# Performance work log

Hardware: AMD Instinct MI355X
Metric: run time of the kernel (lower is better)

## Reference

```python
import jax, jax.numpy as jnp
import numpy as np

DIM = 1024
HEADS = 16
DIM_HEAD = 64
SEQ = 2048
BATCH = 4
BASE = 10000.0
SCALING = 1.0


def rope_cos_sin(seq_len, dim_head, base=BASE, scaling=SCALING):
    inv_freq = scaling / (base ** (jnp.arange(0, dim_head, 2, dtype=jnp.float32) / dim_head))
    t = jnp.arange(seq_len, dtype=jnp.float32)
    freqs = t[:, None] * inv_freq[None, :]            # [S, d/2]
    emb = jnp.concatenate([freqs, freqs], axis=-1)    # [S, d]
    return jnp.cos(emb), jnp.sin(emb)


def apply_rotary(x, cos, sin):
    # x: [B, H, S, d]; cos/sin: [S, d]
    d2 = x.shape[-1] // 2
    c = cos[None, None, :, :d2]
    s = sin[None, None, :, :d2]
    x1, x2 = x[..., :d2], x[..., d2:]
    return jnp.concatenate([x1 * c - x2 * s, x1 * s + x2 * c], axis=-1)


def setup_inputs() -> dict:
    key = jax.random.key(0)
    ks = jax.random.split(key, 5)
    x = jax.random.normal(ks[0], (BATCH, SEQ, DIM), dtype=jnp.float32)
    inner = HEADS * DIM_HEAD
    w_qkv = jax.random.normal(ks[1], (DIM, inner * 3), dtype=jnp.float32) * (DIM ** -0.5)
    w_out = jax.random.normal(ks[2], (inner, DIM), dtype=jnp.float32) * (inner ** -0.5)
    b_out = jnp.zeros((DIM,), dtype=jnp.float32)
    ln_gamma = jnp.ones((DIM,), dtype=jnp.float32)
    ln_beta = jnp.zeros((DIM,), dtype=jnp.float32)
    return {"x": x, "w_qkv": w_qkv, "w_out": w_out, "b_out": b_out,
            "ln_gamma": ln_gamma, "ln_beta": ln_beta}


def reference(x, w_qkv, w_out, b_out, ln_gamma, ln_beta):
    # LayerNorm
    mu = jnp.mean(x, axis=-1, keepdims=True)
    var = jnp.var(x, axis=-1, keepdims=True)
    xn = (x - mu) * jax.lax.rsqrt(var + 1e-5) * ln_gamma + ln_beta
    # QKV projection (no bias)
    qkv = xn @ w_qkv                                  # [B, S, 3*inner]
    q, k, v = jnp.split(qkv, 3, axis=-1)
    def split_heads(t):
        B, S, _ = t.shape
        return t.reshape(B, S, HEADS, DIM_HEAD).transpose(0, 2, 1, 3)
    q, k, v = split_heads(q), split_heads(k), split_heads(v)  # [B, H, S, d]
    cos, sin = rope_cos_sin(SEQ, DIM_HEAD)
    q = apply_rotary(q, cos, sin)
    k = apply_rotary(k, cos, sin)
    scale = DIM_HEAD ** -0.5
    dots = jnp.einsum('bhid,bhjd->bhij', q, k) * scale  # [B, H, S, S]
    attn = jax.nn.softmax(dots, axis=-1)
    out = jnp.einsum('bhij,bhjd->bhid', attn, v)       # [B, H, S, d]
    B, H, S, d = out.shape
    out = out.transpose(0, 2, 1, 3).reshape(B, S, H * d)
    return out @ w_out + b_out
```

## Files before the change

### kernel.cpp

```cpp
#include <hip/hip_runtime.h>
#include <hip/hip_bf16.h>
#include <math.h>

#define B_ 4
#define S_ 2048
#define D_ 1024
#define H_ 16
#define DH_ 64
#define INNER_ 1024
#define N3_ 3072
#define ROWS_ 8192

typedef __attribute__((ext_vector_type(8))) short short8;
typedef __attribute__((ext_vector_type(8))) _Float16 half8;
typedef __attribute__((ext_vector_type(4))) float f32x4;

#define QSCALE_ (0.125f * 1.44269504088896f)

#if __has_builtin(__builtin_amdgcn_exp2f)
#define EXP2N(x) __builtin_amdgcn_exp2f(x)
#else
#define EXP2N(x) exp2f(x)
#endif

__device__ __forceinline__ ushort f16rne(float x) {
    _Float16 h = (_Float16)x;
    return *reinterpret_cast<ushort*>(&h);
}

__device__ __forceinline__ int swz(int row, int colByte) {
    return row * 128 + (colByte ^ ((row & 7) << 4));
}

__device__ __forceinline__ void xcd_remap(int& bx, int& by) {
    const int gx  = gridDim.x;
    const int nwg = gx * gridDim.y;
    const int bid = blockIdx.y * gx + blockIdx.x;
    const int swzid = (bid & 7) * (nwg >> 3) + (bid >> 3);
    bx = swzid % gx;
    by = swzid / gx;
}

__global__ __launch_bounds__(256) void ln_kernel(const float* __restrict__ x,
                                                 const float* __restrict__ gamma,
                                                 const float* __restrict__ beta,
                                                 ushort* __restrict__ xn_f) {
    const int row = blockIdx.x;
    const int tid = threadIdx.x;
    const float4 v = ((const float4*)(x + (size_t)row * D_))[tid];
    float s  = v.x + v.y + v.z + v.w;
    float ss = v.x * v.x + v.y * v.y + v.z * v.z + v.w * v.w;
    #pragma unroll
    for (int off = 32; off > 0; off >>= 1) {
        s  += __shfl_down(s, off);
        ss += __shfl_down(ss, off);
    }
    __shared__ float red[8];
    const int wave = tid >> 6, lane = tid & 63;
    if (lane == 0) { red[wave] = s; red[4 + wave] = ss; }
    __syncthreads();
    const float S  = red[0] + red[1] + red[2] + red[3];
    const float SS = red[4] + red[5] + red[6] + red[7];
    const float mu  = S * (1.0f / D_);
    const float var = SS * (1.0f / D_) - mu * mu;
    const float rs  = rsqrtf(var + 1e-5f);
    const float4 g  = ((const float4*)gamma)[tid];
    const float4 bb = ((const float4*)beta)[tid];
    const float o0 = (v.x - mu) * rs * g.x + bb.x;
    const float o1 = (v.y - mu) * rs * g.y + bb.y;
    const float o2 = (v.z - mu) * rs * g.z + bb.z;
    const float o3 = (v.w - mu) * rs * g.w + bb.w;
    *(ushort4*)(xn_f + (size_t)row * D_ + tid * 4) =
        make_ushort4(f16rne(o0), f16rne(o1), f16rne(o2), f16rne(o3));
}

__global__ __launch_bounds__(256) void wtrans_kernel(const float* __restrict__ W,
                                                     ushort* __restrict__ Tf,
                                                     int K, int N) {
    __shared__ float tile[64][68];
    const int tid = threadIdx.x;
    const int n0 = blockIdx.x * 64, k0 = blockIdx.y * 64;
    const int kr = tid >> 4, nc = (tid & 15) * 4;
    #pragma unroll
    for (int li = 0; li < 4; ++li) {
        const int k = kr + li * 16;
        *(float4*)&tile[k][nc] = *(const float4*)(W + (size_t)(k0 + k) * N + n0 + nc);
    }
    __syncthreads();
    const int nl = tid >> 2;
    const int ks = (tid & 3) * 16;
    ushort hbuf[16];
    #pragma unroll
    for (int i = 0; i < 16; ++i) hbuf[i] = f16rne(tile[ks + i][nl]);
    ushort* th = Tf + (size_t)(n0 + nl) * K + k0 + ks;
    #pragma unroll
    for (int i = 0; i < 4; ++i)
        *(ushort4*)(th + i * 4) = make_ushort4(hbuf[i*4], hbuf[i*4+1], hbuf[i*4+2], hbuf[i*4+3]);
}

__global__ __launch_bounds__(256) void gemm_f16_kernel(
        const ushort* __restrict__ Af, const ushort* __restrict__ Bf,
        float* __restrict__ C, int M, int N, int K,
        const float* __restrict__ bias) {
    __shared__ __align__(16) ushort As[128 * 64];
    __shared__ __align__(16) ushort Bs[128 * 64];
    const int tid  = threadIdx.x;
    const int lane = tid & 63;
    const int wv   = tid >> 6;
    const int lr = lane & 15, lg = lane >> 4;
    const int wr = wv >> 1, wc = wv & 1;
    int bx, by;
    xcd_remap(bx, by);
    const int m0 = by * 128, n0 = bx * 128;

    f32x4 acc[4][4];
    #pragma unroll
    for (int i = 0; i < 4; ++i)
        #pragma unroll
        for (int j = 0; j < 4; ++j) acc[i][j] = (f32x4){0.f, 0.f, 0.f, 0.f};

    const int sr = tid >> 3;
    const int ss = (tid & 7) * 16;

    for (int k0 = 0; k0 < K; k0 += 64) {
        __syncthreads();
        #pragma unroll
        for (int li = 0; li < 4; ++li) {
            const int r = sr + li * 32;
            const int off = swz(r, ss);
            *(uint4*)((char*)As + off) = *(const uint4*)(Af + (size_t)(m0 + r) * K + k0 + (ss >> 1));
            *(uint4*)((char*)Bs + off) = *(const uint4*)(Bf + (size_t)(n0 + r) * K + k0 + (ss >> 1));
        }
        __syncthreads();
        #pragma unroll
        for (int kc = 0; kc < 2; ++kc) {
            const int cb = kc * 64 + lg * 16;
            half8 a[4], b[4];
            #pragma unroll
            for (int i = 0; i < 4; ++i) {
                a[i] = *(half8*)((char*)As + swz(wr * 64 + i * 16 + lr, cb));
                b[i] = *(half8*)((char*)Bs + swz(wc * 64 + i * 16 + lr, cb));
            }
            __builtin_amdgcn_s_setprio(1);
            #pragma unroll
            for (int mi = 0; mi < 4; ++mi)
                #pragma unroll
                for (int ni = 0; ni < 4; ++ni)
                    acc[mi][ni] = __builtin_amdgcn_mfma_f32_16x16x32_f16(a[mi], b[ni], acc[mi][ni], 0, 0, 0);
            __builtin_amdgcn_s_setprio(0);
        }
    }

    #pragma unroll
    for (int mi = 0; mi < 4; ++mi) {
        #pragma unroll
        for (int rr = 0; rr < 4; ++rr) {
            const int row = m0 + wr * 64 + mi * 16 + lg * 4 + rr;
            float* crow = C + (size_t)row * N + n0 + wc * 64;
            #pragma unroll
            for (int ni = 0; ni < 4; ++ni) {
                const int col = ni * 16 + lr;
                float v = acc[mi][ni][rr];
                if (bias) v += bias[n0 + wc * 64 + col];
                crow[col] = v;
            }
        }
    }
}

__global__ __launch_bounds__(256) void gemm_qkv_rope_kernel(
        const ushort* __restrict__ Af, const ushort* __restrict__ Bf,
        ushort* __restrict__ qkv16, int M, int N, int K,
        const float* __restrict__ cost, const float* __restrict__ sint) {
    __shared__ __align__(16) ushort As[128 * 64];
    __shared__ __align__(16) ushort Bs[128 * 64];
    const int tid  = threadIdx.x;
    const int lane = tid & 63;
    const int wv   = tid >> 6;
    const int lr = lane & 15, lg = lane >> 4;
    const int wr = wv >> 1, wc = wv & 1;
    int bx, by;
    xcd_remap(bx, by);
    const int m0 = by * 128, n0 = bx * 128;

    f32x4 acc[4][4];
    #pragma unroll
    for (int i = 0; i < 4; ++i)
        #pragma unroll
        for (int j = 0; j < 4; ++j) acc[i][j] = (f32x4){0.f, 0.f, 0.f, 0.f};

    const int sr = tid >> 3;
    const int ss = (tid & 7) * 16;

    for (int k0 = 0; k0 < K; k0 += 64) {
        __syncthreads();
        #pragma unroll
        for (int li = 0; li < 4; ++li) {
            const int r = sr + li * 32;
            const int off = swz(r, ss);
            *(uint4*)((char*)As + off) = *(const uint4*)(Af + (size_t)(m0 + r) * K + k0 + (ss >> 1));
            *(uint4*)((char*)Bs + off) = *(const uint4*)(Bf + (size_t)(n0 + r) * K + k0 + (ss >> 1));
        }
        __syncthreads();
        #pragma unroll
        for (int kc = 0; kc < 2; ++kc) {
            const int cb = kc * 64 + lg * 16;
            half8 a[4], b[4];
            #pragma unroll
            for (int i = 0; i < 4; ++i) {
                a[i] = *(half8*)((char*)As + swz(wr * 64 + i * 16 + lr, cb));
                b[i] = *(half8*)((char*)Bs + swz(wc * 64 + i * 16 + lr, cb));
            }
            __builtin_amdgcn_s_setprio(1);
            #pragma unroll
            for (int mi = 0; mi < 4; ++mi)
                #pragma unroll
                for (int ni = 0; ni < 4; ++ni)
                    acc[mi][ni] = __builtin_amdgcn_mfma_f32_16x16x32_f16(a[mi], b[ni], acc[mi][ni], 0, 0, 0);
            __builtin_amdgcn_s_setprio(0);
        }
    }

    const int seg = n0 >> 10;
    const int colbase = (n0 & 1023) + wc * 64;
    #pragma unroll
    for (int mi = 0; mi < 4; ++mi) {
        #pragma unroll
        for (int rr = 0; rr < 4; ++rr) {
            const int row = m0 + wr * 64 + mi * 16 + lg * 4 + rr;
            const int spos = row & (S_ - 1);
            ushort* wrow = qkv16 + (size_t)row * 3072 + seg * 1024 + colbase;
            if (seg < 2) {
                #pragma unroll
                for (int p = 0; p < 2; ++p) {
                    const int d2 = p * 16 + lr;
                    const float c = cost[spos * 32 + d2];
                    const float s = sint[spos * 32 + d2];
                    const float v1 = acc[mi][p][rr];
                    const float v2 = acc[mi][p + 2][rr];
                    float r1 = v1 * c - v2 * s;
                    float r2 = v1 * s + v2 * c;
                    if (seg == 0) { r1 *= QSCALE_; r2 *= QSCALE_; }
                    wrow[p * 16 + lr]      = f16rne(r1);
                    wrow[p * 16 + lr + 32] = f16rne(r2);
                }
            } else {
                #pragma unroll
                for (int ni = 0; ni < 4; ++ni)
                    wrow[ni * 16 + lr] = f16rne(acc[mi][ni][rr]);
            }
        }
    }
}

__global__ __launch_bounds__(256) void rope_table_kernel(float* __restrict__ cost,
                                                         float* __restrict__ sint) {
    const int idx = blockIdx.x * 256 + threadIdx.x;
    const int s = idx >> 5;
    const int i = idx & 31;
    const float inv = powf(10000.0f, -(2.0f * (float)i) / 64.0f);
    const float f = (float)s * inv;
    float sv, cv;
    sincosf(f, &sv, &cv);
    cost[idx] = cv;
    sint[idx] = sv;
}

__global__ __launch_bounds__(256) void attn_mfma_kernel(const ushort* __restrict__ Q16,
                                                        ushort* __restrict__ att_f) {
    __shared__ __align__(16) ushort sK[64 * 64];
    __shared__ __align__(16) ushort sV[64 * 64];
    __shared__ __align__(16) ushort Pb[4][2][16 * 64];

    const int tid  = threadIdx.x;
    const int lane = tid & 63;
    const int wv   = tid >> 6;
    const int lr   = lane & 15;
    const int lg   = lane >> 4;

    const int bh = blockIdx.x;
    const int b  = bh >> 4;
    const int h  = bh & 15;
    const int q0 = blockIdx.y * 128;

    half8 q[2][2];
    #pragma unroll
    for (int qt = 0; qt < 2; ++qt) {
        const int qrow = q0 + wv * 32 + qt * 16 + lr;
        const ushort* qp = Q16 + (size_t)(b * S_ + qrow) * 3072 + h * 64;
        #pragma unroll
        for (int kc = 0; kc < 2; ++kc)
            q[qt][kc] = *(const half8*)(qp + kc * 32 + lg * 8);
    }

    half8 onesf;
    #pragma unroll
    for (int i = 0; i < 8; ++i) onesf[i] = (lr == 0) ? (_Float16)1.0f : (_Float16)0.0f;

    f32x4 accO[2][4];
    #pragma unroll
    for (int qt = 0; qt < 2; ++qt)
        #pragma unroll
        for (int t = 0; t < 4; ++t) accO[qt][t] = (f32x4){0.f, 0.f, 0.f, 0.f};
    f32x4 accL[2];
    accL[0] = (f32x4){0.f, 0.f, 0.f, 0.f};
    accL[1] = (f32x4){0.f, 0.f, 0.f, 0.f};

    const int kr0 = tid >> 3, ksl = tid & 7;
    const int vjp = tid & 31;
    const int vd  = (tid >> 5) * 8;

    const ushort* kvbase = Q16 + (size_t)(b * S_) * 3072 + h * 64;

    short8 rk0, rk1, rv0, rv1;

#define LOADT(J0)                                                              \
    {                                                                          \
        const ushort* ktb = kvbase + (size_t)(J0) * 3072 + 1024;               \
        rk0 = *(const short8*)(ktb + (size_t)kr0 * 3072 + ksl * 8);            \
        rk1 = *(const short8*)(ktb + (size_t)(kr0 + 32) * 3072 + ksl * 8);     \
        const ushort* vtb = kvbase + (size_t)(J0) * 3072 + 2048;               \
        rv0 = *(const short8*)(vtb + (size_t)(2 * vjp) * 3072 + vd);           \
        rv1 = *(const short8*)(vtb + (size_t)(2 * vjp + 1) * 3072 + vd);       \
    }

#define WRITET()                                                               \
    {                                                                          \
        *(short8*)((char*)sK + swz(kr0, ksl * 16)) = rk0;                      \
        *(short8*)((char*)sK + swz(kr0 + 32, ksl * 16)) = rk1;                 \
        _Pragma("unroll")                                                      \
        for (int i = 0; i < 8; ++i) {                                          \
            const int off = swz(vd + i, vjp * 4);                              \
            *(uint*)((char*)sV + off) = (uint)(ushort)rv0[i] | ((uint)(ushort)rv1[i] << 16); \
        }                                                                      \
    }

    LOADT(0)
    WRITET()

    const int NT = S_ / 64;
    for (int t = 0; t < NT; ++t) {
        __syncthreads();
        if (t + 1 < NT) LOADT((t + 1) * 64)

        f32x4 accS[2][4];
        #pragma unroll
        for (int qt = 0; qt < 2; ++qt)
            #pragma unroll
            for (int tt = 0; tt < 4; ++tt) accS[qt][tt] = (f32x4){0.f, 0.f, 0.f, 0.f};
        #pragma unroll
        for (int kc = 0; kc < 2; ++kc) {
            #pragma unroll
            for (int tt = 0; tt < 4; ++tt) {
                const int off = swz(tt * 16 + lr, (kc * 32 + lg * 8) * 2);
                half8 kv = *(half8*)((char*)sK + off);
                #pragma unroll
                for (int qt = 0; qt < 2; ++qt)
                    accS[qt][tt] = __builtin_amdgcn_mfma_f32_16x16x32_f16(q[qt][kc], kv, accS[qt][tt], 0, 0, 0);
            }
        }

        #pragma unroll
        for (int qt = 0; qt < 2; ++qt) {
            #pragma unroll
            for (int tt = 0; tt < 4; ++tt)
                #pragma unroll
                for (int r = 0; r < 4; ++r) {
                    const float pv = EXP2N(accS[qt][tt][r]);
                    const int off = swz(lg * 4 + r, (tt * 16 + lr) * 2);
                    *(ushort*)((char*)Pb[wv][qt] + off) = f16rne(pv);
                }
        }

        #pragma unroll
        for (int jc = 0; jc < 2; ++jc) {
            const int aoff = swz(lr, (jc * 32 + lg * 8) * 2);
            half8 pa0 = *(half8*)((char*)Pb[wv][0] + aoff);
            half8 pa1 = *(half8*)((char*)Pb[wv][1] + aoff);
            accL[0] = __builtin_amdgcn_mfma_f32_16x16x32_f16(pa0, onesf, accL[0], 0, 0, 0);
            accL[1] = __builtin_amdgcn_mfma_f32_16x16x32_f16(pa1, onesf, accL[1], 0, 0, 0);
            #pragma unroll
            for (int dt = 0; dt < 4; ++dt) {
                const int boff = swz(dt * 16 + lr, (jc * 32 + lg * 8) * 2);
                half8 vvf = *(half8*)((char*)sV + boff);
                accO[0][dt] = __builtin_amdgcn_mfma_f32_16x16x32_f16(pa0, vvf, accO[0][dt], 0, 0, 0);
                accO[1][dt] = __builtin_amdgcn_mfma_f32_16x16x32_f16(pa1, vvf, accO[1][dt], 0, 0, 0);
            }
        }

        __syncthreads();
        if (t + 1 < NT) WRITET()
    }

    #pragma unroll
    for (int qt = 0; qt < 2; ++qt) {
        #pragma unroll
        for (int r = 0; r < 4; ++r) {
            const float L = __shfl(accL[qt][r], lane & 48);
            const float inv_l = 1.0f / L;
            const int q_ = q0 + wv * 32 + qt * 16 + lg * 4 + r;
            const size_t ob = ((size_t)(b * S_ + q_)) * INNER_ + h * 64;
            #pragma unroll
            for (int dt = 0; dt < 4; ++dt)
                att_f[ob + dt * 16 + lr] = f16rne(accO[qt][dt][r] * inv_l);
        }
    }
#undef LOADT
#undef WRITET
}

extern "C" void kernel_launch(void* const* d_in, const int* in_sizes, int n_in,
                              void* d_out, int out_size, void* d_ws, size_t ws_size,
                              hipStream_t stream) {
    const float* x        = (const float*)d_in[0];
    const float* w_qkv    = (const float*)d_in[1];
    const float* w_out    = (const float*)d_in[2];
    const float* b_out    = (const float*)d_in[3];
    const float* ln_gamma = (const float*)d_in[4];
    const float* ln_beta  = (const float*)d_in[5];
    float* out = (float*)d_out;

    char* wsb = (char*)d_ws;
    ushort* qkv16 = (ushort*)wsb;
    ushort* xn_f  = (ushort*)(wsb + 100663296);
    ushort* att_f = xn_f;
    ushort* wqT_f = (ushort*)(wsb + 134217728);
    ushort* woT_f = (ushort*)(wsb + 134217728 + 8388608);
    float*  cost  = (float*)(wsb + 146800640);
    float*  sint  = cost + S_ * 32;

    ln_kernel<<<ROWS_, 256, 0, stream>>>(x, ln_gamma, ln_beta, xn_f);

    wtrans_kernel<<<dim3(N3_ / 64, D_ / 64), 256, 0, stream>>>(w_qkv, wqT_f, D_, N3_);
    rope_table_kernel<<<(S_ * 32) / 256, 256, 0, stream>>>(cost, sint);

    gemm_qkv_rope_kernel<<<dim3(N3_ / 128, ROWS_ / 128), 256, 0, stream>>>(
        xn_f, wqT_f, qkv16, ROWS_, N3_, D_, cost, sint);

    attn_mfma_kernel<<<dim3(B_ * H_, S_ / 128), 256, 0, stream>>>(qkv16, att_f);

    wtrans_kernel<<<dim3(D_ / 64, D_ / 64), 256, 0, stream>>>(w_out, woT_f, D_, D_);

    gemm_f16_kernel<<<dim3(D_ / 128, ROWS_ / 128), 256, 0, stream>>>(
        att_f, woT_f, out, ROWS_, D_, INNER_, b_out);
}
```

Baseline: 254.5 us.

## Keep attention probabilities in registers by computing transposed S via swapped MFMA operands

After: 235.8 us. 7.3% less time.

```diff
diff --git a/kernel.cpp b/kernel.cpp
--- a/kernel.cpp
+++ b/kernel.cpp
@@ -13,6 +13,7 @@
 
 typedef __attribute__((ext_vector_type(8))) short short8;
 typedef __attribute__((ext_vector_type(8))) _Float16 half8;
+typedef __attribute__((ext_vector_type(4))) _Float16 half4;
 typedef __attribute__((ext_vector_type(4))) float f32x4;
 
 #define QSCALE_ (0.125f * 1.44269504088896f)
@@ -270,7 +271,6 @@
                                                         ushort* __restrict__ att_f) {
     __shared__ __align__(16) ushort sK[64 * 64];
     __shared__ __align__(16) ushort sV[64 * 64];
-    __shared__ __align__(16) ushort Pb[4][2][16 * 64];
 
     const int tid  = threadIdx.x;
     const int lane = tid & 63;
@@ -293,18 +293,12 @@
             q[qt][kc] = *(const half8*)(qp + kc * 32 + lg * 8);
     }
 
-    half8 onesf;
-    #pragma unroll
-    for (int i = 0; i < 8; ++i) onesf[i] = (lr == 0) ? (_Float16)1.0f : (_Float16)0.0f;
-
     f32x4 accO[2][4];
     #pragma unroll
     for (int qt = 0; qt < 2; ++qt)
         #pragma unroll
         for (int t = 0; t < 4; ++t) accO[qt][t] = (f32x4){0.f, 0.f, 0.f, 0.f};
-    f32x4 accL[2];
-    accL[0] = (f32x4){0.f, 0.f, 0.f, 0.f};
-    accL[1] = (f32x4){0.f, 0.f, 0.f, 0.f};
+    float lrun[2] = {0.f, 0.f};
 
     const int kr0 = tid >> 3, ksl = tid & 7;
     const int vjp = tid & 31;
@@ -356,35 +350,37 @@
                 half8 kv = *(half8*)((char*)sK + off);
                 #pragma unroll
                 for (int qt = 0; qt < 2; ++qt)
-                    accS[qt][tt] = __builtin_amdgcn_mfma_f32_16x16x32_f16(q[qt][kc], kv, accS[qt][tt], 0, 0, 0);
-            }
-        }
-
+                    accS[qt][tt] = __builtin_amdgcn_mfma_f32_16x16x32_f16(kv, q[qt][kc], accS[qt][tt], 0, 0, 0);
+            }
+        }
+
+        half4 pf[2][4];
         #pragma unroll
         for (int qt = 0; qt < 2; ++qt) {
-            #pragma unroll
-            for (int tt = 0; tt < 4; ++tt)
-                #pragma unroll
-                for (int r = 0; r < 4; ++r) {
-                    const float pv = EXP2N(accS[qt][tt][r]);
-                    const int off = swz(lg * 4 + r, (tt * 16 + lr) * 2);
-                    *(ushort*)((char*)Pb[wv][qt] + off) = f16rne(pv);
-                }
-        }
-
-        #pragma unroll
-        for (int jc = 0; jc < 2; ++jc) {
-            const int aoff = swz(lr, (jc * 32 + lg * 8) * 2);
-            half8 pa0 = *(half8*)((char*)Pb[wv][0] + aoff);
-            half8 pa1 = *(half8*)((char*)Pb[wv][1] + aoff);
-            accL[0] = __builtin_amdgcn_mfma_f32_16x16x32_f16(pa0, onesf, accL[0], 0, 0, 0);
-            accL[1] = __builtin_amdgcn_mfma_f32_16x16x32_f16(pa1, onesf, accL[1], 0, 0, 0);
+            float ls = 0.f;
+            #pragma unroll
+            for (int tt = 0; tt < 4; ++tt) {
+                const float p0 = EXP2N(accS[qt][tt][0]);
+                const float p1 = EXP2N(accS[qt][tt][1]);
+                const float p2 = EXP2N(accS[qt][tt][2]);
+                const float p3 = EXP2N(accS[qt][tt][3]);
+                ls += (p0 + p1) + (p2 + p3);
+                half4 pk;
+                pk[0] = (_Float16)p0; pk[1] = (_Float16)p1;
+                pk[2] = (_Float16)p2; pk[3] = (_Float16)p3;
+                pf[qt][tt] = pk;
+            }
+            lrun[qt] += ls;
+        }
+
+        #pragma unroll
+        for (int tt = 0; tt < 4; ++tt) {
             #pragma unroll
             for (int dt = 0; dt < 4; ++dt) {
-                const int boff = swz(dt * 16 + lr, (jc * 32 + lg * 8) * 2);
-                half8 vvf = *(half8*)((char*)sV + boff);
-                accO[0][dt] = __builtin_amdgcn_mfma_f32_16x16x32_f16(pa0, vvf, accO[0][dt], 0, 0, 0);
-                accO[1][dt] = __builtin_amdgcn_mfma_f32_16x16x32_f16(pa1, vvf, accO[1][dt], 0, 0, 0);
+                const int boff = swz(dt * 16 + lr, (tt * 16 + lg * 4) * 2);
+                half4 vv = *(half4*)((char*)sV + boff);
+                accO[0][dt] = __builtin_amdgcn_mfma_f32_16x16x16f16(pf[0][tt], vv, accO[0][dt], 0, 0, 0);
+                accO[1][dt] = __builtin_amdgcn_mfma_f32_16x16x16f16(pf[1][tt], vv, accO[1][dt], 0, 0, 0);
             }
         }
 
@@ -392,11 +388,20 @@
         if (t + 1 < NT) WRITET()
     }
 
+    float Lq[2];
     #pragma unroll
     for (int qt = 0; qt < 2; ++qt) {
+        float L = lrun[qt];
+        L += __shfl_xor(L, 16);
+        L += __shfl_xor(L, 32);
+        Lq[qt] = L;
+    }
+
+    #pragma unroll
+    for (int qt = 0; qt < 2; ++qt) {
         #pragma unroll
         for (int r = 0; r < 4; ++r) {
-            const float L = __shfl(accL[qt][r], lane & 48);
+            const float L = __shfl(Lq[qt], lg * 4 + r);
             const float inv_l = 1.0f / L;
             const int q_ = q0 + wv * 32 + qt * 16 + lg * 4 + r;
             const size_t ob = ((size_t)(b * S_ + q_)) * INNER_ + h * 64;
```
